# Kernel optimization log

Hardware: AMD Instinct MI355X
Metric: run time of the kernel (lower is better)

Reference implementation:

```python
import jax, jax.numpy as jnp
import numpy as np

HE, WE, L = 361, 720, 37   # ERA5 source grid (0.5 deg) and pressure levels
HM, WM, K = 180, 360, 32   # model grid (1 deg) and model sigma levels
EPS = 1e-8

# ERA5 standard 37 pressure levels in Pa (ascending)
P_LEVELS = [100., 200., 300., 500., 700., 1000., 2000., 3000., 5000., 7000.,
            10000., 12500., 15000., 17500., 20000., 22500., 25000., 30000.,
            35000., 40000., 45000., 50000., 55000., 60000., 65000., 70000.,
            75000., 77500., 80000., 82500., 85000., 87500., 90000., 92500.,
            95000., 97500., 100000.]


def setup_inputs() -> dict:
    key = jax.random.key(0)
    ks = jax.random.split(key, 6)
    u = 10.0 * jax.random.normal(ks[0], (HE, WE, L), jnp.float32)
    v = 10.0 * jax.random.normal(ks[1], (HE, WE, L), jnp.float32)
    w = 0.1 * jax.random.normal(ks[2], (HE, WE, L), jnp.float32)
    T = 250.0 + 30.0 * jax.random.normal(ks[3], (HE, WE, L), jnp.float32)
    q = 0.01 * jax.random.uniform(ks[4], (HE, WE, L), jnp.float32)
    ps = 95000.0 + 5000.0 * jax.random.normal(ks[5], (HE, WE), jnp.float32)
    era5_lat = jnp.linspace(-90.0, 90.0, HE, dtype=jnp.float32)
    era5_lon = jnp.linspace(0.0, 359.5, WE, dtype=jnp.float32)
    model_lat = jnp.linspace(-89.0, 89.0, HM, dtype=jnp.float32)
    model_lon = jnp.linspace(0.25, 359.75, WM, dtype=jnp.float32)
    p_levels = jnp.asarray(P_LEVELS, jnp.float32)
    b_k = ((jnp.arange(K, dtype=jnp.float32) + 0.5) / K)
    a_k = 100.0 * (1.0 - b_k)  # simple hybrid coefficients (Pa)
    return dict(u=u, v=v, w=w, T=T, q=q, ps=ps,
                era5_lat=era5_lat, era5_lon=era5_lon,
                model_lat=model_lat, model_lon=model_lon,
                p_levels=p_levels, a_k=a_k, b_k=b_k)


def _axis_interp(grid, pts):
    """1D linear interp indices/weights with linear extrapolation (fill_value=None)."""
    i = jnp.clip(jnp.searchsorted(grid, pts, side='right') - 1, 0, grid.shape[0] - 2)
    t = (pts - grid[i]) / (grid[i + 1] - grid[i])
    return i, t


def _forward(u, v, w, T, q, ps, era5_lat, era5_lon, model_lat, model_lon,
             p_levels, a_k, b_k):
    # ---- horizontal bilinear interp (RegularGridInterpolator, linear) ----
    stacked = jnp.concatenate([u, v, w, T, q, ps[..., None]], axis=-1)  # [HE,WE,5L+1]
    iy, ty = _axis_interp(era5_lat, model_lat)   # [HM]
    ix, tx = _axis_interp(era5_lon, model_lon)   # [WM]
    r0 = stacked[iy]       # [HM,WE,C]
    r1 = stacked[iy + 1]
    d00, d01 = r0[:, ix], r0[:, ix + 1]          # [HM,WM,C]
    d10, d11 = r1[:, ix], r1[:, ix + 1]
    wy = ty[:, None, None]
    wx = tx[None, :, None]
    hd = (1 - wy) * ((1 - wx) * d00 + wx * d01) + wy * ((1 - wx) * d10 + wx * d11)
    vars_h = hd[..., :5 * L].reshape(HM, WM, 5, L)  # [HM,WM,5,L]
    ps_m = hd[..., -1]                               # [HM,WM]

    # ---- model pressure: p = a_k + b_k * ps ----
    p_model = a_k + b_k * ps_m[..., None]            # [HM,WM,K]

    # ---- vertical log-pressure linear interp with per-pixel valid mask ----
    logp_e = jnp.log(p_levels + EPS)                 # [L]
    logp_m = jnp.log(p_model + EPS)                  # [HM,WM,K]
    nvalid = jnp.searchsorted(p_levels, ps_m, side='right')  # levels with p<=ps
    idx = jnp.searchsorted(logp_e, logp_m, side='right') - 1
    idx = jnp.clip(idx, 0, jnp.maximum(nvalid[..., None] - 2, 0))  # [HM,WM,K]
    x0, x1 = logp_e[idx], logp_e[idx + 1]
    t = (logp_m - x0) / (x1 - x0)                    # linear extrapolation at edges
    g0 = jnp.take_along_axis(vars_h, idx[:, :, None, :], axis=3)        # [HM,WM,5,K]
    g1 = jnp.take_along_axis(vars_h, (idx + 1)[:, :, None, :], axis=3)
    out = g0 + t[:, :, None, :] * (g1 - g0)
    out = jnp.where(nvalid[:, :, None, None] >= 2, out, 0.0)            # <2 valid -> 0

    # ---- unit conversion / clamps ----
    u_o, v_o, w_o = out[:, :, 0], out[:, :, 1], out[:, :, 2]
    T_o = jnp.clip(out[:, :, 3], 150.0, 350.0)
    q_o = jnp.clip(out[:, :, 4], 0.0, 0.05)
    ps_o = jnp.clip(ps_m, 30000.0, 110000.0)
    out3d = jnp.stack([u_o, v_o, w_o, T_o, q_o], axis=-1)  # [HM,WM,K,5]
    return out3d, p_model, ps_o


def reference(u, v, w, T, q, ps, era5_lat, era5_lon, model_lat, model_lon,
              p_levels, a_k, b_k):
    return _forward(u, v, w, T, q, ps, era5_lat, era5_lon,
                    model_lat, model_lon, p_levels, a_k, b_k)
```

## Files before the change

kernel.cpp:

```cpp
#include <hip/hip_runtime.h>
#include <cmath>

#define HE 361
#define WE 720
#define LL 37
#define HM 180
#define WM 360
#define KK 32
#define NPTS (HM * WM)
#define EPSF 1e-8f
#define PTSB 8
#define WE37 (WE * LL)

#define OFF1 ((size_t)HM * WM * KK * 5)
#define OFF2 (OFF1 + (size_t)HM * WM * KK)

#define WS_IY    0
#define WS_TY    180
#define WS_IX    360
#define WS_TX    720
#define WS_LOGPE 1080

__device__ __forceinline__ int upper_bound_g(const float* a, int n, float v) {
    int lo = 0, hi = n;
    while (lo < hi) {
        int m = (lo + hi) >> 1;
        if (a[m] <= v) lo = m + 1; else hi = m;
    }
    return lo;
}

__global__ void precompute_kernel(const float* __restrict__ era5_lat,
                                  const float* __restrict__ era5_lon,
                                  const float* __restrict__ model_lat,
                                  const float* __restrict__ model_lon,
                                  const float* __restrict__ p_levels,
                                  int* __restrict__ ws_iy, float* __restrict__ ws_ty,
                                  int* __restrict__ ws_ix, float* __restrict__ ws_tx,
                                  float* __restrict__ ws_logpe) {
    int t = blockIdx.x * blockDim.x + threadIdx.x;
    if (t < HM) {
        float v = model_lat[t];
        int i = upper_bound_g(era5_lat, HE, v) - 1;
        if (i < 0) i = 0;
        if (i > HE - 2) i = HE - 2;
        ws_iy[t] = i;
        ws_ty[t] = (v - era5_lat[i]) / (era5_lat[i + 1] - era5_lat[i]);
    } else if (t < HM + WM) {
        int j = t - HM;
        float v = model_lon[j];
        int i = upper_bound_g(era5_lon, WE, v) - 1;
        if (i < 0) i = 0;
        if (i > WE - 2) i = WE - 2;
        ws_ix[j] = i;
        ws_tx[j] = (v - era5_lon[i]) / (era5_lon[i + 1] - era5_lon[i]);
    } else if (t < HM + WM + LL) {
        int k = t - HM - WM;
        ws_logpe[k] = logf(p_levels[k] + EPSF);
    }
}

__global__ void __launch_bounds__(256)
fused_kernel(const float* __restrict__ u, const float* __restrict__ v,
             const float* __restrict__ w, const float* __restrict__ T,
             const float* __restrict__ q, const float* __restrict__ ps,
             const float* __restrict__ p_levels,
             const float* __restrict__ a_k, const float* __restrict__ b_k,
             const int* __restrict__ ws_iy, const float* __restrict__ ws_ty,
             const int* __restrict__ ws_ix, const float* __restrict__ ws_tx,
             const float* __restrict__ ws_logpe,
             float* __restrict__ out) {
    __shared__ float s_h[PTSB][5 * LL];
    __shared__ float s_psm[PTSB];
    __shared__ int   s_maxi[PTSB];
    __shared__ int   s_inval[PTSB];
    __shared__ float s_logpe[4][LL];
    __shared__ float s_out[4][2 * KK * 5];

    const int tid      = threadIdx.x;
    const int wv       = tid >> 6;
    const int lane     = tid & 63;
    const int pt_local = tid >> 5;
    const int grp      = tid & 31;

    if (lane < LL) s_logpe[wv][lane] = ws_logpe[lane];

    const int y  = (blockIdx.x * PTSB) / WM;
    const int x0 = blockIdx.x * PTSB - y * WM;
    const int x  = x0 + pt_local;
    const int pt = blockIdx.x * PTSB + pt_local;

    const int   iy = ws_iy[y];
    const float ty = ws_ty[y];
    const int   ix = ws_ix[x];
    const float tx = ws_tx[x];
    const float omty = 1.0f - ty;
    const float omtx = 1.0f - tx;

    const int b00  = iy * WE + ix;
    const int base = b00 * LL;
    const int i0   = base + grp;
    const int i1   = base + grp + WE37;

    float a00[5], a01[5], a10[5], a11[5];
#define LD4(slot, S) \
    a00[slot] = S[i0];      a01[slot] = S[i0 + LL]; \
    a10[slot] = S[i1];      a11[slot] = S[i1 + LL];
    LD4(0, u) LD4(1, v) LD4(2, w) LD4(3, T) LD4(4, q)
#undef LD4

    const bool tval = (grp < 25);
    int tvar = grp / 5;
    int tl   = 32 + (grp - tvar * 5);
    if (!tval) { tvar = 0; tl = 32; }
    const float* ts = (tvar == 0) ? u : (tvar == 1) ? v
                    : (tvar == 2) ? w : (tvar == 3) ? T : q;
    const int ti0 = base + tl;
    const int ti1 = base + tl + WE37;
    const float t00 = ts[ti0], t01 = ts[ti0 + LL];
    const float t10 = ts[ti1], t11 = ts[ti1 + LL];

    const float ak = a_k[grp];
    const float bk = b_k[grp];

    if (grp == 0) {
        const float p00 = ps[b00], p01 = ps[b00 + 1];
        const float p10 = ps[b00 + WE], p11 = ps[b00 + WE + 1];
        const float ps_m = omty * (omtx * p00 + tx * p01) + ty * (omtx * p10 + tx * p11);
        s_psm[pt_local] = ps_m;
        const int nvalid = upper_bound_g(p_levels, LL, ps_m);
        int maxi = nvalid - 2;
        if (maxi < 0) maxi = 0;
        s_maxi[pt_local]  = maxi;
        s_inval[pt_local] = (nvalid < 2) ? 1 : 0;
        out[OFF2 + pt] = fminf(fmaxf(ps_m, 30000.0f), 110000.0f);
    }

#pragma unroll
    for (int it = 0; it < 5; it++) {
        const float hv = omty * (omtx * a00[it] + tx * a01[it]) +
                         ty   * (omtx * a10[it] + tx * a11[it]);
        s_h[pt_local][it * LL + grp] = hv;
    }
    {
        const float hv = omty * (omtx * t00 + tx * t01) + ty * (omtx * t10 + tx * t11);
        if (tval) s_h[pt_local][tvar * LL + tl] = hv;
    }

    const int   k       = grp;
    const float ps_m    = s_psm[pt_local];
    const int   maxi    = s_maxi[pt_local];
    const bool  invalid = (s_inval[pt_local] != 0);

    const float pm = ak + bk * ps_m;
    out[OFF1 + (size_t)pt * KK + k] = pm;

    const float lpm = logf(pm + EPSF);
    int lo = 0, hi = LL;
    while (lo < hi) {
        int m = (lo + hi) >> 1;
        if (s_logpe[wv][m] <= lpm) lo = m + 1; else hi = m;
    }
    int i = lo - 1;
    if (i < 0) i = 0;
    if (i > maxi) i = maxi;
    const float t = (lpm - s_logpe[wv][i]) / (s_logpe[wv][i + 1] - s_logpe[wv][i]);

    const int half = lane >> 5;
    float* so = &s_out[wv][half * (KK * 5)];
#pragma unroll
    for (int var = 0; var < 5; var++) {
        const float g0 = s_h[pt_local][var * LL + i];
        const float g1 = s_h[pt_local][var * LL + i + 1];
        float o = g0 + t * (g1 - g0);
        if (invalid) o = 0.0f;
        if (var == 3) o = fminf(fmaxf(o, 150.0f), 350.0f);
        if (var == 4) o = fminf(fmaxf(o, 0.0f), 0.05f);
        so[k * 5 + var] = o;
    }

    __builtin_amdgcn_wave_barrier();

    const size_t ob = (size_t)(blockIdx.x * PTSB + 2 * wv) * (KK * 5);
#pragma unroll
    for (int c = 0; c < 5; c++) {
        out[ob + lane + 64 * c] = s_out[wv][lane + 64 * c];
    }
}

extern "C" void kernel_launch(void* const* d_in, const int* in_sizes, int n_in,
                              void* d_out, int out_size, void* d_ws, size_t ws_size,
                              hipStream_t stream) {
    const float* u         = (const float*)d_in[0];
    const float* v         = (const float*)d_in[1];
    const float* w         = (const float*)d_in[2];
    const float* T         = (const float*)d_in[3];
    const float* q         = (const float*)d_in[4];
    const float* ps        = (const float*)d_in[5];
    const float* era5_lat  = (const float*)d_in[6];
    const float* era5_lon  = (const float*)d_in[7];
    const float* model_lat = (const float*)d_in[8];
    const float* model_lon = (const float*)d_in[9];
    const float* p_levels  = (const float*)d_in[10];
    const float* a_k       = (const float*)d_in[11];
    const float* b_k       = (const float*)d_in[12];

    float* wsf = (float*)d_ws;
    int*   ws_iy    = (int*)(wsf + WS_IY);
    float* ws_ty    = wsf + WS_TY;
    int*   ws_ix    = (int*)(wsf + WS_IX);
    float* ws_tx    = wsf + WS_TX;
    float* ws_logpe = wsf + WS_LOGPE;

    float* out = (float*)d_out;

    precompute_kernel<<<3, 256, 0, stream>>>(era5_lat, era5_lon, model_lat, model_lon,
                                             p_levels, ws_iy, ws_ty, ws_ix, ws_tx,
                                             ws_logpe);

    const int blocks = NPTS / PTSB;
    fused_kernel<<<blocks, 256, 0, stream>>>(u, v, w, T, q, ps, p_levels, a_k, b_k,
                                             ws_iy, ws_ty, ws_ix, ws_tx, ws_logpe, out);
}
```

Before: 232.9 us.

## Process four tiles per block with double-buffered register prefetch and linear level search

Each block now handles four 8-point tiles and issues the global loads for the next tile before consuming the current one, using two register sets and two shared buffers. Every lane computes the surface-pressure interpolation itself, and a fully unrolled linear count over a shared (p, logp) table replaces the single-lane binary search and the shared broadcast. The aim is to hide global-load latency and remove the serial branchy searches. The cost is a quarter as many blocks and higher register pressure, which may lower occupancy.

```diff
diff --git a/kernel.cpp b/kernel.cpp
--- a/kernel.cpp
+++ b/kernel.cpp
@@ -10,6 +10,7 @@
 #define NPTS (HM * WM)
 #define EPSF 1e-8f
 #define PTSB 8
+#define TPB  4
 #define WE37 (WE * LL)
 
 #define OFF1 ((size_t)HM * WM * KK * 5)
@@ -60,6 +61,138 @@
     }
 }
 
+struct Geo { int b00; int pt; float tx, ty; };
+
+struct LSet {
+    float a00[5], a01[5], a10[5], a11[5];
+    float t00, t01, t10, t11;
+    float p00, p01, p10, p11;
+};
+
+__device__ __forceinline__ Geo geom_load(int tt, int pt_local,
+                                         const int* __restrict__ ws_iy,
+                                         const float* __restrict__ ws_ty,
+                                         const int* __restrict__ ws_ix,
+                                         const float* __restrict__ ws_tx) {
+    Geo g;
+    g.pt = tt * PTSB + pt_local;
+    const int y = g.pt / WM;
+    const int x = g.pt - y * WM;
+    const int iy = ws_iy[y];
+    const int ix = ws_ix[x];
+    g.ty = ws_ty[y];
+    g.tx = ws_tx[x];
+    g.b00 = iy * WE + ix;
+    return g;
+}
+
+__device__ __forceinline__ void issue_loads(const Geo& g, int grp,
+                                            const float* __restrict__ u,
+                                            const float* __restrict__ v,
+                                            const float* __restrict__ w,
+                                            const float* __restrict__ T,
+                                            const float* __restrict__ q,
+                                            const float* __restrict__ ps,
+                                            LSet& s) {
+    const int base = g.b00 * LL;
+    const int i0 = base + grp;
+    const int i1 = i0 + WE37;
+#define LD4(slot, S) \
+    s.a00[slot] = S[i0];  s.a01[slot] = S[i0 + LL]; \
+    s.a10[slot] = S[i1];  s.a11[slot] = S[i1 + LL];
+    LD4(0, u) LD4(1, v) LD4(2, w) LD4(3, T) LD4(4, q)
+#undef LD4
+    int tvar = grp / 5;
+    int tl   = 32 + (grp - tvar * 5);
+    if (grp >= 25) { tvar = 0; tl = 32; }
+    const float* ts = (tvar == 0) ? u : (tvar == 1) ? v
+                    : (tvar == 2) ? w : (tvar == 3) ? T : q;
+    const int ti0 = base + tl;
+    const int ti1 = ti0 + WE37;
+    s.t00 = ts[ti0]; s.t01 = ts[ti0 + LL];
+    s.t10 = ts[ti1]; s.t11 = ts[ti1 + LL];
+    s.p00 = ps[g.b00];      s.p01 = ps[g.b00 + 1];
+    s.p10 = ps[g.b00 + WE]; s.p11 = ps[g.b00 + WE + 1];
+}
+
+template <int BUF>
+__device__ __forceinline__ void consume(const Geo& g, const LSet& s, int tt,
+                                        int wv, int lane, int pt_local, int grp,
+                                        float ak, float bk,
+                                        const float2 (*s_tab)[LL],
+                                        float (*s_h)[PTSB][5 * LL],
+                                        float (*s_out)[2 * KK * 5],
+                                        float* __restrict__ out) {
+    const float ty = g.ty, tx = g.tx;
+    const float omty = 1.0f - ty, omtx = 1.0f - tx;
+
+#pragma unroll
+    for (int it = 0; it < 5; it++) {
+        const float hv = omty * (omtx * s.a00[it] + tx * s.a01[it]) +
+                         ty   * (omtx * s.a10[it] + tx * s.a11[it]);
+        s_h[BUF][pt_local][it * LL + grp] = hv;
+    }
+    {
+        const float hv = omty * (omtx * s.t00 + tx * s.t01) +
+                         ty   * (omtx * s.t10 + tx * s.t11);
+        if (grp < 25) {
+            const int tvar = grp / 5;
+            const int tl   = 32 + (grp - tvar * 5);
+            s_h[BUF][pt_local][tvar * LL + tl] = hv;
+        }
+    }
+
+    const float ps_m = omty * (omtx * s.p00 + tx * s.p01) +
+                       ty   * (omtx * s.p10 + tx * s.p11);
+    if (grp == 0) out[OFF2 + g.pt] = fminf(fmaxf(ps_m, 30000.0f), 110000.0f);
+
+    const float pm = ak + bk * ps_m;
+    out[OFF1 + (size_t)g.pt * KK + grp] = pm;
+
+    const float lpm = logf(pm + EPSF);
+
+    int nv = 0, ii = 0;
+#pragma unroll
+    for (int m = 0; m < LL; m++) {
+        const float2 tb = s_tab[wv][m];
+        nv += (tb.x <= ps_m) ? 1 : 0;
+        if (m >= 1) ii += (tb.y <= lpm) ? 1 : 0;
+    }
+    int maxi = nv - 2;
+    if (maxi < 0) maxi = 0;
+    if (ii > maxi) ii = maxi;
+    const bool invalid = (nv < 2);
+
+    const float x0 = s_tab[wv][ii].y;
+    const float x1 = s_tab[wv][ii + 1].y;
+    const float t = (lpm - x0) / (x1 - x0);
+
+    __builtin_amdgcn_wave_barrier();
+
+    const int half = lane >> 5;
+    float* so = &s_out[wv][half * (KK * 5)];
+#pragma unroll
+    for (int var = 0; var < 5; var++) {
+        const float g0 = s_h[BUF][pt_local][var * LL + ii];
+        const float g1 = s_h[BUF][pt_local][var * LL + ii + 1];
+        float o = g0 + t * (g1 - g0);
+        if (invalid) o = 0.0f;
+        if (var == 3) o = fminf(fmaxf(o, 150.0f), 350.0f);
+        if (var == 4) o = fminf(fmaxf(o, 0.0f), 0.05f);
+        so[grp * 5 + var] = o;
+    }
+
+    __builtin_amdgcn_wave_barrier();
+
+    const size_t ob = (size_t)(tt * PTSB + 2 * wv) * (KK * 5);
+#pragma unroll
+    for (int c = 0; c < 5; c++) {
+        out[ob + lane + 64 * c] = s_out[wv][lane + 64 * c];
+    }
+
+    __builtin_amdgcn_wave_barrier();
+}
+
 __global__ void __launch_bounds__(256)
 fused_kernel(const float* __restrict__ u, const float* __restrict__ v,
              const float* __restrict__ w, const float* __restrict__ T,
@@ -70,12 +203,9 @@
              const int* __restrict__ ws_ix, const float* __restrict__ ws_tx,
              const float* __restrict__ ws_logpe,
              float* __restrict__ out) {
-    __shared__ float s_h[PTSB][5 * LL];
-    __shared__ float s_psm[PTSB];
-    __shared__ int   s_maxi[PTSB];
-    __shared__ int   s_inval[PTSB];
-    __shared__ float s_logpe[4][LL];
-    __shared__ float s_out[4][2 * KK * 5];
+    __shared__ float2 s_tab[4][LL];
+    __shared__ float  s_h[2][PTSB][5 * LL];
+    __shared__ float  s_out[4][2 * KK * 5];
 
     const int tid      = threadIdx.x;
     const int wv       = tid >> 6;
@@ -83,109 +213,27 @@
     const int pt_local = tid >> 5;
     const int grp      = tid & 31;
 
-    if (lane < LL) s_logpe[wv][lane] = ws_logpe[lane];
-
-    const int y  = (blockIdx.x * PTSB) / WM;
-    const int x0 = blockIdx.x * PTSB - y * WM;
-    const int x  = x0 + pt_local;
-    const int pt = blockIdx.x * PTSB + pt_local;
-
-    const int   iy = ws_iy[y];
-    const float ty = ws_ty[y];
-    const int   ix = ws_ix[x];
-    const float tx = ws_tx[x];
-    const float omty = 1.0f - ty;
-    const float omtx = 1.0f - tx;
-
-    const int b00  = iy * WE + ix;
-    const int base = b00 * LL;
-    const int i0   = base + grp;
-    const int i1   = base + grp + WE37;
-
-    float a00[5], a01[5], a10[5], a11[5];
-#define LD4(slot, S) \
-    a00[slot] = S[i0];      a01[slot] = S[i0 + LL]; \
-    a10[slot] = S[i1];      a11[slot] = S[i1 + LL];
-    LD4(0, u) LD4(1, v) LD4(2, w) LD4(3, T) LD4(4, q)
-#undef LD4
-
-    const bool tval = (grp < 25);
-    int tvar = grp / 5;
-    int tl   = 32 + (grp - tvar * 5);
-    if (!tval) { tvar = 0; tl = 32; }
-    const float* ts = (tvar == 0) ? u : (tvar == 1) ? v
-                    : (tvar == 2) ? w : (tvar == 3) ? T : q;
-    const int ti0 = base + tl;
-    const int ti1 = base + tl + WE37;
-    const float t00 = ts[ti0], t01 = ts[ti0 + LL];
-    const float t10 = ts[ti1], t11 = ts[ti1 + LL];
+    if (lane < LL) s_tab[wv][lane] = make_float2(p_levels[lane], ws_logpe[lane]);
 
     const float ak = a_k[grp];
     const float bk = b_k[grp];
 
-    if (grp == 0) {
-        const float p00 = ps[b00], p01 = ps[b00 + 1];
-        const float p10 = ps[b00 + WE], p11 = ps[b00 + WE + 1];
-        const float ps_m = omty * (omtx * p00 + tx * p01) + ty * (omtx * p10 + tx * p11);
-        s_psm[pt_local] = ps_m;
-        const int nvalid = upper_bound_g(p_levels, LL, ps_m);
-        int maxi = nvalid - 2;
-        if (maxi < 0) maxi = 0;
-        s_maxi[pt_local]  = maxi;
-        s_inval[pt_local] = (nvalid < 2) ? 1 : 0;
-        out[OFF2 + pt] = fminf(fmaxf(ps_m, 30000.0f), 110000.0f);
-    }
-
-#pragma unroll
-    for (int it = 0; it < 5; it++) {
-        const float hv = omty * (omtx * a00[it] + tx * a01[it]) +
-                         ty   * (omtx * a10[it] + tx * a11[it]);
-        s_h[pt_local][it * LL + grp] = hv;
-    }
-    {
-        const float hv = omty * (omtx * t00 + tx * t01) + ty * (omtx * t10 + tx * t11);
-        if (tval) s_h[pt_local][tvar * LL + tl] = hv;
-    }
-
-    const int   k       = grp;
-    const float ps_m    = s_psm[pt_local];
-    const int   maxi    = s_maxi[pt_local];
-    const bool  invalid = (s_inval[pt_local] != 0);
-
-    const float pm = ak + bk * ps_m;
-    out[OFF1 + (size_t)pt * KK + k] = pm;
-
-    const float lpm = logf(pm + EPSF);
-    int lo = 0, hi = LL;
-    while (lo < hi) {
-        int m = (lo + hi) >> 1;
-        if (s_logpe[wv][m] <= lpm) lo = m + 1; else hi = m;
-    }
-    int i = lo - 1;
-    if (i < 0) i = 0;
-    if (i > maxi) i = maxi;
-    const float t = (lpm - s_logpe[wv][i]) / (s_logpe[wv][i + 1] - s_logpe[wv][i]);
-
-    const int half = lane >> 5;
-    float* so = &s_out[wv][half * (KK * 5)];
-#pragma unroll
-    for (int var = 0; var < 5; var++) {
-        const float g0 = s_h[pt_local][var * LL + i];
-        const float g1 = s_h[pt_local][var * LL + i + 1];
-        float o = g0 + t * (g1 - g0);
-        if (invalid) o = 0.0f;
-        if (var == 3) o = fminf(fmaxf(o, 150.0f), 350.0f);
-        if (var == 4) o = fminf(fmaxf(o, 0.0f), 0.05f);
-        so[k * 5 + var] = o;
-    }
-
-    __builtin_amdgcn_wave_barrier();
-
-    const size_t ob = (size_t)(blockIdx.x * PTSB + 2 * wv) * (KK * 5);
-#pragma unroll
-    for (int c = 0; c < 5; c++) {
-        out[ob + lane + 64 * c] = s_out[wv][lane + 64 * c];
-    }
+    const int tt0 = blockIdx.x * TPB;
+    const Geo g0 = geom_load(tt0 + 0, pt_local, ws_iy, ws_ty, ws_ix, ws_tx);
+    const Geo g1 = geom_load(tt0 + 1, pt_local, ws_iy, ws_ty, ws_ix, ws_tx);
+    const Geo g2 = geom_load(tt0 + 2, pt_local, ws_iy, ws_ty, ws_ix, ws_tx);
+    const Geo g3 = geom_load(tt0 + 3, pt_local, ws_iy, ws_ty, ws_ix, ws_tx);
+
+    LSet sA, sB;
+    issue_loads(g0, grp, u, v, w, T, q, ps, sA);
+    issue_loads(g1, grp, u, v, w, T, q, ps, sB);
+
+    consume<0>(g0, sA, tt0 + 0, wv, lane, pt_local, grp, ak, bk, s_tab, s_h, s_out, out);
+    issue_loads(g2, grp, u, v, w, T, q, ps, sA);
+    consume<1>(g1, sB, tt0 + 1, wv, lane, pt_local, grp, ak, bk, s_tab, s_h, s_out, out);
+    issue_loads(g3, grp, u, v, w, T, q, ps, sB);
+    consume<0>(g2, sA, tt0 + 2, wv, lane, pt_local, grp, ak, bk, s_tab, s_h, s_out, out);
+    consume<1>(g3, sB, tt0 + 3, wv, lane, pt_local, grp, ak, bk, s_tab, s_h, s_out, out);
 }
 
 extern "C" void kernel_launch(void* const* d_in, const int* in_sizes, int n_in,
@@ -218,7 +266,7 @@
                                              p_levels, ws_iy, ws_ty, ws_ix, ws_tx,
                                              ws_logpe);
 
-    const int blocks = NPTS / PTSB;
+    const int blocks = NPTS / (PTSB * TPB);
     fused_kernel<<<blocks, 256, 0, stream>>>(u, v, w, T, q, ps, p_levels, a_k, b_k,
                                              ws_iy, ws_ty, ws_ix, ws_tx, ws_logpe, out);
 }
```

New measurement: 235.4 us. About the same (+1.1%).

## Stage source rows into LDS via direct global-to-LDS loads and unroll level search

Applied to the files above, without the earlier changes.

Each block now cooperatively copies the contiguous source row spans covering its 8 output points (two latitude rows, up to 16 longitude columns, five variables) into shared memory with 16-byte direct global-to-LDS loads. Horizontal interpolation then reads from shared memory instead of issuing scattered per-thread global loads. Each lane also recomputes the surface pressure and replaces the binary searches with an unrolled linear scan over a combined pressure/log-pressure table, which removes the single-thread section. The cost is a block-wide barrier, about 24KB of extra shared memory that can limit occupancy, and a column cap of 16 that assumes a narrow footprint.

```diff
diff --git a/kernel.cpp b/kernel.cpp
--- a/kernel.cpp
+++ b/kernel.cpp
@@ -1,5 +1,6 @@
 #include <hip/hip_runtime.h>
 #include <cmath>
+#include <stdint.h>
 
 #define HE 361
 #define WE 720
@@ -20,6 +21,12 @@
 #define WS_IX    360
 #define WS_TX    720
 #define WS_LOGPE 1080
+
+#define RSTR 150
+#define RFL  600
+#define NRANGE 10
+#define NSLOT (RSTR * NRANGE)
+#define NROUND 6
 
 __device__ __forceinline__ int upper_bound_g(const float* a, int n, float v) {
     int lo = 0, hi = n;
@@ -70,12 +77,10 @@
              const int* __restrict__ ws_ix, const float* __restrict__ ws_tx,
              const float* __restrict__ ws_logpe,
              float* __restrict__ out) {
-    __shared__ float s_h[PTSB][5 * LL];
-    __shared__ float s_psm[PTSB];
-    __shared__ int   s_maxi[PTSB];
-    __shared__ int   s_inval[PTSB];
-    __shared__ float s_logpe[4][LL];
-    __shared__ float s_out[4][2 * KK * 5];
+    __shared__ float  s_stage[NRANGE * RFL];
+    __shared__ float  s_h[PTSB][5 * LL];
+    __shared__ float2 s_tab[4][LL];
+    __shared__ float  s_out[4][2 * KK * 5];
 
     const int tid      = threadIdx.x;
     const int wv       = tid >> 6;
@@ -83,105 +88,126 @@
     const int pt_local = tid >> 5;
     const int grp      = tid & 31;
 
-    if (lane < LL) s_logpe[wv][lane] = ws_logpe[lane];
-
-    const int y  = (blockIdx.x * PTSB) / WM;
-    const int x0 = blockIdx.x * PTSB - y * WM;
-    const int x  = x0 + pt_local;
-    const int pt = blockIdx.x * PTSB + pt_local;
+    if (lane < LL) s_tab[wv][lane] = make_float2(p_levels[lane], ws_logpe[lane]);
+
+    const int pt0 = blockIdx.x * PTSB;
+    const int y   = pt0 / WM;
+    const int x0  = pt0 - y * WM;
+    const int x   = x0 + pt_local;
+    const int pt  = pt0 + pt_local;
 
     const int   iy = ws_iy[y];
     const float ty = ws_ty[y];
+    const int   c0 = ws_ix[x0];
     const int   ix = ws_ix[x];
     const float tx = ws_tx[x];
-    const float omty = 1.0f - ty;
-    const float omtx = 1.0f - tx;
-
-    const int b00  = iy * WE + ix;
-    const int base = b00 * LL;
-    const int i0   = base + grp;
-    const int i1   = base + grp + WE37;
-
-    float a00[5], a01[5], a10[5], a11[5];
-#define LD4(slot, S) \
-    a00[slot] = S[i0];      a01[slot] = S[i0 + LL]; \
-    a10[slot] = S[i1];      a11[slot] = S[i1 + LL];
-    LD4(0, u) LD4(1, v) LD4(2, w) LD4(3, T) LD4(4, q)
-#undef LD4
-
-    const bool tval = (grp < 25);
-    int tvar = grp / 5;
-    int tl   = 32 + (grp - tvar * 5);
-    if (!tval) { tvar = 0; tl = 32; }
-    const float* ts = (tvar == 0) ? u : (tvar == 1) ? v
-                    : (tvar == 2) ? w : (tvar == 3) ? T : q;
-    const int ti0 = base + tl;
-    const int ti1 = base + tl + WE37;
-    const float t00 = ts[ti0], t01 = ts[ti0 + LL];
-    const float t10 = ts[ti1], t11 = ts[ti1 + LL];
+
+    int ncols = ws_ix[x0 + PTSB - 1] + 2 - c0;
+    if (ncols > 16) ncols = 16;
+    const int crel = ix - c0;
+
+    const int se0 = (iy * WE + c0) * LL;
+    const int se1 = se0 + WE37;
+    const int h0  = se0 & 3, h1 = se1 & 3;
+    const int f00 = se0 - h0, f01 = se1 - h1;
+    const int n40 = (h0 + ncols * LL + 3) >> 2;
+    const int n41 = (h1 + ncols * LL + 3) >> 2;
+
+#pragma unroll
+    for (int k = 0; k < NROUND; k++) {
+        const int slot = tid + 256 * k;
+        if (slot < NSLOT) {
+            const int r  = slot / RSTR;
+            const int c  = slot - r * RSTR;
+            const int rr = r & 1;
+            const int vv = r >> 1;
+            const int n4 = rr ? n41 : n40;
+            if (c < n4) {
+                const int fbase = (rr ? f01 : f00) + 4 * c;
+                const float* gp = ((vv == 0) ? u : (vv == 1) ? v
+                                  : (vv == 2) ? w : (vv == 3) ? T : q) + fbase;
+                float* lp = &s_stage[r * RFL + 4 * c];
+                __builtin_amdgcn_global_load_lds(
+                    (const __attribute__((address_space(1))) void*)gp,
+                    (__attribute__((address_space(3))) void*)lp, 16, 0, 0);
+            }
+        }
+    }
+
+    const int b00 = iy * WE + ix;
+    const float p00 = ps[b00], p01 = ps[b00 + 1];
+    const float p10 = ps[b00 + WE], p11 = ps[b00 + WE + 1];
 
     const float ak = a_k[grp];
     const float bk = b_k[grp];
 
-    if (grp == 0) {
-        const float p00 = ps[b00], p01 = ps[b00 + 1];
-        const float p10 = ps[b00 + WE], p11 = ps[b00 + WE + 1];
-        const float ps_m = omty * (omtx * p00 + tx * p01) + ty * (omtx * p10 + tx * p11);
-        s_psm[pt_local] = ps_m;
-        const int nvalid = upper_bound_g(p_levels, LL, ps_m);
-        int maxi = nvalid - 2;
-        if (maxi < 0) maxi = 0;
-        s_maxi[pt_local]  = maxi;
-        s_inval[pt_local] = (nvalid < 2) ? 1 : 0;
-        out[OFF2 + pt] = fminf(fmaxf(ps_m, 30000.0f), 110000.0f);
-    }
-
-#pragma unroll
-    for (int it = 0; it < 5; it++) {
-        const float hv = omty * (omtx * a00[it] + tx * a01[it]) +
-                         ty   * (omtx * a10[it] + tx * a11[it]);
-        s_h[pt_local][it * LL + grp] = hv;
-    }
-    {
-        const float hv = omty * (omtx * t00 + tx * t01) + ty * (omtx * t10 + tx * t11);
-        if (tval) s_h[pt_local][tvar * LL + tl] = hv;
-    }
-
-    const int   k       = grp;
-    const float ps_m    = s_psm[pt_local];
-    const int   maxi    = s_maxi[pt_local];
-    const bool  invalid = (s_inval[pt_local] != 0);
+    __syncthreads();
+
+    const float omty = 1.0f - ty, omtx = 1.0f - tx;
+    const int   cb   = crel * LL;
+
+#pragma unroll
+    for (int vv = 0; vv < 5; vv++) {
+        const float* r0 = &s_stage[(vv * 2 + 0) * RFL + h0 + cb];
+        const float* r1 = &s_stage[(vv * 2 + 1) * RFL + h1 + cb];
+        const float d00 = r0[grp], d01 = r0[grp + LL];
+        const float d10 = r1[grp], d11 = r1[grp + LL];
+        s_h[pt_local][vv * LL + grp] =
+            omty * (omtx * d00 + tx * d01) + ty * (omtx * d10 + tx * d11);
+    }
+    if (grp < 25) {
+        const int tvar = grp / 5;
+        const int tl   = 32 + (grp - tvar * 5);
+        const float* r0 = &s_stage[(tvar * 2 + 0) * RFL + h0 + cb];
+        const float* r1 = &s_stage[(tvar * 2 + 1) * RFL + h1 + cb];
+        const float d00 = r0[tl], d01 = r0[tl + LL];
+        const float d10 = r1[tl], d11 = r1[tl + LL];
+        s_h[pt_local][tvar * LL + tl] =
+            omty * (omtx * d00 + tx * d01) + ty * (omtx * d10 + tx * d11);
+    }
+
+    const float ps_m = omty * (omtx * p00 + tx * p01) + ty * (omtx * p10 + tx * p11);
+    if (grp == 0) out[OFF2 + pt] = fminf(fmaxf(ps_m, 30000.0f), 110000.0f);
 
     const float pm = ak + bk * ps_m;
-    out[OFF1 + (size_t)pt * KK + k] = pm;
+    out[OFF1 + (size_t)pt * KK + grp] = pm;
 
     const float lpm = logf(pm + EPSF);
-    int lo = 0, hi = LL;
-    while (lo < hi) {
-        int m = (lo + hi) >> 1;
-        if (s_logpe[wv][m] <= lpm) lo = m + 1; else hi = m;
-    }
-    int i = lo - 1;
-    if (i < 0) i = 0;
-    if (i > maxi) i = maxi;
-    const float t = (lpm - s_logpe[wv][i]) / (s_logpe[wv][i + 1] - s_logpe[wv][i]);
+
+    int nv = 0, ii = 0;
+#pragma unroll
+    for (int m = 0; m < LL; m++) {
+        const float2 tb = s_tab[wv][m];
+        nv += (tb.x <= ps_m) ? 1 : 0;
+        if (m >= 1) ii += (tb.y <= lpm) ? 1 : 0;
+    }
+    int maxi = nv - 2;
+    if (maxi < 0) maxi = 0;
+    if (ii > maxi) ii = maxi;
+    const bool invalid = (nv < 2);
+
+    const float lx0 = s_tab[wv][ii].y;
+    const float lx1 = s_tab[wv][ii + 1].y;
+    const float t = (lpm - lx0) / (lx1 - lx0);
+
+    __builtin_amdgcn_wave_barrier();
 
     const int half = lane >> 5;
     float* so = &s_out[wv][half * (KK * 5)];
 #pragma unroll
     for (int var = 0; var < 5; var++) {
-        const float g0 = s_h[pt_local][var * LL + i];
-        const float g1 = s_h[pt_local][var * LL + i + 1];
+        const float g0 = s_h[pt_local][var * LL + ii];
+        const float g1 = s_h[pt_local][var * LL + ii + 1];
         float o = g0 + t * (g1 - g0);
         if (invalid) o = 0.0f;
         if (var == 3) o = fminf(fmaxf(o, 150.0f), 350.0f);
         if (var == 4) o = fminf(fmaxf(o, 0.0f), 0.05f);
-        so[k * 5 + var] = o;
+        so[grp * 5 + var] = o;
     }
 
     __builtin_amdgcn_wave_barrier();
 
-    const size_t ob = (size_t)(blockIdx.x * PTSB + 2 * wv) * (KK * 5);
+    const size_t ob = (size_t)(pt0 + 2 * wv) * (KK * 5);
 #pragma unroll
     for (int c = 0; c < 5; c++) {
         out[ob + lane + 64 * c] = s_out[wv][lane + 64 * c];
```

Measured after the change: 232.9 us. About the same (-0.0%).
